# Optimization experiments

Measured on AMD Instinct MI355X. Metric: run time of the kernel, lower is better.

## Reference

```python
import jax, jax.numpy as jnp
import numpy as np

EPS = 1e-5  # torch BatchNorm1d default eps


def setup_inputs() -> dict:
    key = jax.random.key(0)
    ks = jax.random.split(key, 8)
    F, P = 32, 64            # frames, peds per frame
    B = F * P                # batch = 2048
    E, H, M, D = 64, 128, 512, 1024  # embed, h_dim, pool_mlp_dim, bottleneck
    starts = np.arange(F, dtype=np.int64) * P
    seq_start_end = jnp.asarray(np.stack([starts, starts + P], axis=1))
    inp = {
        "curr_h_states": jax.random.normal(ks[0], (1, B, H), dtype=jnp.float32),
        "curr_pos": jax.random.normal(ks[1], (B, 2), dtype=jnp.float32),
        "seq_start_end": seq_start_end,
        # embedding: Linear(2, E)
        "We": jax.random.normal(ks[2], (2, E), dtype=jnp.float32) * 0.5,
        "be": jnp.zeros((E,), dtype=jnp.float32),
        # mlp layer 1: Linear(E+H, M) + BN(M)
        "W1": jax.random.normal(ks[3], (E + H, M), dtype=jnp.float32) * 0.05,
        "b1": jnp.zeros((M,), dtype=jnp.float32),
        "g1": jnp.ones((M,), dtype=jnp.float32),
        "beta1": jnp.zeros((M,), dtype=jnp.float32),
        # mlp layer 2: Linear(M, D) + BN(D)
        "W2": jax.random.normal(ks[4], (M, D), dtype=jnp.float32) * 0.04,
        "b2": jnp.zeros((D,), dtype=jnp.float32),
        "g2": jnp.ones((D,), dtype=jnp.float32),
        "beta2": jnp.zeros((D,), dtype=jnp.float32),
        # BN running stats (eval mode)
        "rm1": jnp.zeros((M,), dtype=jnp.float32),
        "rv1": jnp.ones((M,), dtype=jnp.float32),
        "rm2": jnp.zeros((D,), dtype=jnp.float32),
        "rv2": jnp.ones((D,), dtype=jnp.float32),
    }
    return inp


def _bn(x, g, beta, rm, rv):
    return g * (x - rm) * jax.lax.rsqrt(rv + EPS) + beta


def reference(curr_h_states, curr_pos, seq_start_end, We, be, W1, b1, g1, beta1,
              W2, b2, g2, beta2, rm1, rv1, rm2, rv2):
    # Equal-size frames: vectorize the per-frame Python loop via a reshape.
    F = seq_start_end.shape[0]
    B = curr_h_states.shape[1]
    P = B // F
    h = curr_h_states[0].reshape(F, P, -1)      # (F, P, H)
    pos = curr_pos.reshape(F, P, 2)             # (F, P, 2)
    # rel_pos[f, i, j] = pos[f, j] - pos[f, i]  (repeat minus repeat_interleave)
    rel = pos[:, None, :, :] - pos[:, :, None, :]          # (F, P, P, 2)
    emb = rel @ We + be                                     # (F, P, P, E)
    h_rep = jnp.broadcast_to(h[:, None, :, :], (F, P, P, h.shape[-1]))
    x = jnp.concatenate([emb, h_rep], axis=-1)              # (F, P, P, E+H)
    x = jax.nn.relu(_bn(x @ W1 + b1, g1, beta1, rm1, rv1))  # (F, P, P, M)
    x = jax.nn.relu(_bn(x @ W2 + b2, g2, beta2, rm2, rv2))  # (F, P, P, D)
    pool_h = x.max(axis=2)                                  # max over j -> (F, P, D)
    return pool_h.reshape(B, -1)                            # (B, D)
```

## Files before the change

kernel.cpp:

```cpp
#include <hip/hip_runtime.h>
#include <hip/hip_bf16.h>
#include <stdint.h>

#define EPS_BN 1e-5f

constexpr int Fn = 32;
constexpr int Pn = 64;
constexpr int Bn = 2048;
constexpr int Hn = 128;
constexpr int En = 64;
constexpr int Mn = 512;
constexpr int Dn = 1024;

using bf16x8  = __attribute__((ext_vector_type(8))) short;
using f32x16  = __attribute__((ext_vector_type(16))) float;

static __device__ __forceinline__ float    bcf(uint32_t u) { return __builtin_bit_cast(float, u); }
static __device__ __forceinline__ uint32_t bcu(float f)    { return __builtin_bit_cast(uint32_t, f); }
static __device__ __forceinline__ unsigned short bfbits(float f) {
  return __builtin_bit_cast(unsigned short, __float2bfloat16(f));
}

static __device__ __forceinline__ void dma16(const uint4* g, uint4* l) {
  __builtin_amdgcn_global_load_lds(
      (const __attribute__((address_space(1))) unsigned int*)g,
      (__attribute__((address_space(3))) unsigned int*)l, 16, 0, 0);
}

static __device__ __forceinline__ bf16x8 mk_af(uint4 a, uint4 q) {
  uint4 x;
#pragma unroll
  for (int v = 0; v < 4; ++v) {
    uint32_t aw = ((const uint32_t*)&a)[v], qw = ((const uint32_t*)&q)[v];
    float lo = fmaxf(bcf(aw << 16) - bcf(qw << 16), 0.f);
    float hi = fmaxf(bcf(aw) - bcf(qw), 0.f);
    ((uint32_t*)&x)[v] = __builtin_amdgcn_perm(bcu(hi), bcu(lo), 0x07060302u);
  }
  return __builtin_bit_cast(bf16x8, x);
}

__global__ void prep_all(const float* __restrict__ hs, const float* __restrict__ pos,
                         const float* __restrict__ We, const float* __restrict__ be,
                         const float* __restrict__ W1, const float* __restrict__ b1,
                         const float* __restrict__ g1, const float* __restrict__ beta1,
                         const float* __restrict__ rm1, const float* __restrict__ rv1,
                         const float* __restrict__ W2, const float* __restrict__ b2,
                         const float* __restrict__ g2, const float* __restrict__ beta2,
                         const float* __restrict__ rm2, const float* __restrict__ rv2,
                         __hip_bfloat16* __restrict__ Agb, __hip_bfloat16* __restrict__ Qgb,
                         uint4* __restrict__ W2g, float* __restrict__ c2) {
  __shared__ float smem[64 * 65];
  int bid = blockIdx.x, t = threadIdx.x;
  if (bid < 512) {
    int rb = bid * 4, m = t;
    float* hsh = smem;
    float* psh = smem + 512;
    if (t < 4 * Hn) hsh[t] = hs[rb * Hn + t];
    if (t < 8) psh[t] = pos[rb * 2 + t];
    __syncthreads();
    float w0 = 0.f, w1 = 0.f, c = 0.f;
    for (int e = 0; e < En; ++e) {
      float w = W1[e * Mn + m];
      w0 += We[e] * w; w1 += We[En + e] * w; c += be[e] * w;
    }
    c += b1[m];
    float s  = g1[m] * rsqrtf(rv1[m] + EPS_BN);
    float tt = beta1[m] - rm1[m] * s;
    float acc[4];
#pragma unroll
    for (int ri = 0; ri < 4; ++ri) acc[ri] = c;
    for (int e = 0; e < Hn; ++e) {
      float w = W1[(En + e) * Mn + m];
#pragma unroll
      for (int ri = 0; ri < 4; ++ri) acc[ri] += hsh[ri * Hn + e] * w;
    }
#pragma unroll
    for (int ri = 0; ri < 4; ++ri) {
      float q = psh[ri * 2] * w0 + psh[ri * 2 + 1] * w1;
      Agb[(rb + ri) * Mn + m] = __float2bfloat16((acc[ri] + q) * s + tt);
      Qgb[(rb + ri) * Mn + m] = __float2bfloat16(q * s);
    }
  } else {
    int b2i = bid - 512;
    int d0 = (b2i & 15) * 64, k0 = (b2i >> 4) * 64;
    int col = t & 63, row8 = t >> 6;
#pragma unroll
    for (int rr = 0; rr < 8; ++rr) {
      int row = rr * 8 + row8;
      smem[row * 65 + col] = W2[(k0 + row) * Dn + d0 + col];
    }
    __syncthreads();
    int lane = t & 63, q8 = t >> 6;
    int sel_n = q8 & 1, sel_ks = q8 >> 1;
    int dl = sel_n * 32 + (lane & 31), d = d0 + dl;
    float sf = g2[d] * rsqrtf(rv2[d] + EPS_BN);
    int kb = sel_ks * 16 + (lane >> 5) * 8;
    uint32_t wd[4];
#pragma unroll
    for (int h = 0; h < 4; ++h) {
      uint32_t u0 = bfbits(smem[(kb + 2 * h) * 65 + dl] * sf);
      uint32_t u1 = bfbits(smem[(kb + 2 * h + 1) * 65 + dl] * sf);
      wd[h] = u0 | (u1 << 16);
    }
    int n32 = (d0 >> 5) + sel_n;
    int ks  = (k0 >> 4) + sel_ks;
    W2g[(n32 * 32 + ks) * 64 + lane] = (uint4){wd[0], wd[1], wd[2], wd[3]};
    if (k0 == 0 && t < 64) {
      int dd = d0 + t;
      float ss = g2[dd] * rsqrtf(rv2[dd] + EPS_BN);
      c2[dd] = b2[dd] * ss + beta2[dd] - rm2[dd] * ss;
    }
  }
}

__launch_bounds__(256, 2)
__global__ void gemm_pool(const __hip_bfloat16* __restrict__ Agb,
                          const __hip_bfloat16* __restrict__ Qgb,
                          const uint4* __restrict__ W2g,
                          const float* __restrict__ c2, float* __restrict__ out) {
  __shared__ uint4 Bs[4096];

  int ct = blockIdx.x;
  int rt = blockIdx.y;
  int f = rt >> 4, i0 = (rt & 15) * 4;

  int t = threadIdx.x, lane = t & 63, w = t >> 6;
  int i = i0 + w;
  int ko = lane >> 5;

  const uint4* aPj0 = (const uint4*)(Agb + (f * Pn + (lane & 31)) * Mn) + ko;
  const uint4* aPj1 = (const uint4*)(Agb + (f * Pn + 32 + (lane & 31)) * Mn) + ko;
  const uint4* qP   = (const uint4*)(Qgb + (f * Pn + i) * Mn) + ko;
  const uint4* W2base = W2g + (size_t)(4 * ct) * 32 * 64 + lane;

  f32x16 acc[2][4];
#pragma unroll
  for (int jf = 0; jf < 2; ++jf)
#pragma unroll
    for (int nf = 0; nf < 4; ++nf)
      acc[jf][nf] = (f32x16){0.f,0.f,0.f,0.f,0.f,0.f,0.f,0.f,0.f,0.f,0.f,0.f,0.f,0.f,0.f,0.f};

  uint4 rA00 = aPj0[0], rA01 = aPj1[0], rQ0 = qP[0];
  uint4 rA10 = aPj0[2], rA11 = aPj1[2], rQ1 = qP[2];

  for (int ph = 0; ph < 2; ++ph) {
    if (ph) __syncthreads();
#pragma unroll
    for (int s = 0; s < 16; ++s) {
      int slot = w * 16 + s;
      int ksl = slot >> 2, nf = slot & 3;
      dma16(W2base + (nf * 32 + ph * 16 + ksl) * 64, Bs + slot * 64);
    }
    __syncthreads();

    for (int kc8 = 0; kc8 < 8; ++kc8) {
      int kc = ph * 8 + kc8;
      int kn = (kc < 15) ? kc + 1 : 15;
      {
        bf16x8 af0 = mk_af(rA00, rQ0);
        bf16x8 af1 = mk_af(rA01, rQ0);
#pragma unroll
        for (int nf = 0; nf < 4; ++nf) {
          bf16x8 bg = *(const bf16x8*)(Bs + ((kc8 * 2 + 0) * 4 + nf) * 64 + lane);
          acc[0][nf] = __builtin_amdgcn_mfma_f32_32x32x16_bf16(af0, bg, acc[0][nf], 0, 0, 0);
          acc[1][nf] = __builtin_amdgcn_mfma_f32_32x32x16_bf16(af1, bg, acc[1][nf], 0, 0, 0);
        }
      }
      rA00 = aPj0[kn * 4]; rA01 = aPj1[kn * 4]; rQ0 = qP[kn * 4];
      {
        bf16x8 af0 = mk_af(rA10, rQ1);
        bf16x8 af1 = mk_af(rA11, rQ1);
#pragma unroll
        for (int nf = 0; nf < 4; ++nf) {
          bf16x8 bg = *(const bf16x8*)(Bs + ((kc8 * 2 + 1) * 4 + nf) * 64 + lane);
          acc[0][nf] = __builtin_amdgcn_mfma_f32_32x32x16_bf16(af0, bg, acc[0][nf], 0, 0, 0);
          acc[1][nf] = __builtin_amdgcn_mfma_f32_32x32x16_bf16(af1, bg, acc[1][nf], 0, 0, 0);
        }
      }
      rA10 = aPj0[kn * 4 + 2]; rA11 = aPj1[kn * 4 + 2]; rQ1 = qP[kn * 4 + 2];
    }
  }

#pragma unroll
  for (int nf = 0; nf < 4; ++nf) {
    float mx = 0.f;
#pragma unroll
    for (int jf = 0; jf < 2; ++jf)
#pragma unroll
      for (int rg = 0; rg < 16; ++rg)
        mx = fmaxf(mx, acc[jf][nf][rg]);
    mx = fmaxf(mx, __shfl_xor(mx, 32));
    if (lane < 32) {
      int d = ct * 128 + nf * 32 + (lane & 31);
      out[(f * Pn + i) * Dn + d] = fmaxf(mx + c2[d], 0.f);
    }
  }
}

extern "C" void kernel_launch(void* const* d_in, const int* in_sizes, int n_in,
                              void* d_out, int out_size, void* d_ws, size_t ws_size,
                              hipStream_t stream) {
  const float* hs    = (const float*)d_in[0];
  const float* pos   = (const float*)d_in[1];
  const float* We    = (const float*)d_in[3];
  const float* be    = (const float*)d_in[4];
  const float* W1    = (const float*)d_in[5];
  const float* b1    = (const float*)d_in[6];
  const float* g1    = (const float*)d_in[7];
  const float* beta1 = (const float*)d_in[8];
  const float* W2    = (const float*)d_in[9];
  const float* b2    = (const float*)d_in[10];
  const float* g2    = (const float*)d_in[11];
  const float* beta2 = (const float*)d_in[12];
  const float* rm1   = (const float*)d_in[13];
  const float* rv1   = (const float*)d_in[14];
  const float* rm2   = (const float*)d_in[15];
  const float* rv2   = (const float*)d_in[16];

  char* ws = (char*)d_ws;
  float* c2 = (float*)(ws + 0);
  __hip_bfloat16* Agb = (__hip_bfloat16*)(ws + 4096);
  __hip_bfloat16* Qgb = (__hip_bfloat16*)(ws + 4096 + 2097152);
  uint4* W2g = (uint4*)(ws + 4096 + 2 * 2097152);
  float* out = (float*)d_out;

  prep_all<<<640, 512, 0, stream>>>(hs, pos, We, be, W1, b1, g1, beta1, rm1, rv1,
                                    W2, b2, g2, beta2, rm2, rv2, Agb, Qgb, W2g, c2);
  gemm_pool<<<dim3(Dn / 128, (Fn * Pn * Pn) / 256), 256, 0, stream>>>(Agb, Qgb, W2g, c2, out);
}
```

Measured before the change: 264.6 us.

## Stage shared A rows in LDS and split W2 loads into four phases

After: 250.5 us. 5.3% less time.

```diff
diff --git a/kernel.cpp b/kernel.cpp
--- a/kernel.cpp
+++ b/kernel.cpp
@@ -21,7 +21,7 @@
   return __builtin_bit_cast(unsigned short, __float2bfloat16(f));
 }
 
-static __device__ __forceinline__ void dma16(const uint4* g, uint4* l) {
+static __device__ __forceinline__ void dma16(const uint4* g, const uint4* l) {
   __builtin_amdgcn_global_load_lds(
       (const __attribute__((address_space(1))) unsigned int*)g,
       (__attribute__((address_space(3))) unsigned int*)l, 16, 0, 0);
@@ -118,7 +118,7 @@
                           const __hip_bfloat16* __restrict__ Qgb,
                           const uint4* __restrict__ W2g,
                           const float* __restrict__ c2, float* __restrict__ out) {
-  __shared__ uint4 Bs[4096];
+  __shared__ uint4 SH[4096];
 
   int ct = blockIdx.x;
   int rt = blockIdx.y;
@@ -126,12 +126,25 @@
 
   int t = threadIdx.x, lane = t & 63, w = t >> 6;
   int i = i0 + w;
-  int ko = lane >> 5;
-
-  const uint4* aPj0 = (const uint4*)(Agb + (f * Pn + (lane & 31)) * Mn) + ko;
-  const uint4* aPj1 = (const uint4*)(Agb + (f * Pn + 32 + (lane & 31)) * Mn) + ko;
-  const uint4* qP   = (const uint4*)(Qgb + (f * Pn + i) * Mn) + ko;
-  const uint4* W2base = W2g + (size_t)(4 * ct) * 32 * 64 + lane;
+
+  const uint4* Au4 = (const uint4*)(Agb + (size_t)f * Pn * Mn);
+  const uint4* aGL = Au4 + (size_t)(lane & 31) * 64 + (lane >> 5);
+  const uint4* bGL = W2g + (size_t)(4 * ct) * 32 * 64 + lane;
+  const uint4* qP = (const uint4*)(Qgb + (size_t)(f * Pn + i) * Mn) + (lane >> 5);
+
+#pragma unroll
+  for (int s = 0; s < 8; ++s) {
+    int sa = w * 8 + s;
+    int kcA = sa >> 2, kst = (sa >> 1) & 1, jf = sa & 1;
+    dma16(aGL + (size_t)jf * 32 * 64 + kcA * 4 + kst * 2, SH + sa * 64);
+  }
+#pragma unroll
+  for (int s = 0; s < 8; ++s) {
+    int sb = w * 8 + s;
+    int kq = sb >> 2, nf = sb & 3;
+    dma16(bGL + (nf * 32 + kq) * 64, SH + 2048 + sb * 64);
+  }
+  uint4 qc0 = qP[0], qc1 = qP[2];
 
   f32x16 acc[2][4];
 #pragma unroll
@@ -140,44 +153,50 @@
     for (int nf = 0; nf < 4; ++nf)
       acc[jf][nf] = (f32x16){0.f,0.f,0.f,0.f,0.f,0.f,0.f,0.f,0.f,0.f,0.f,0.f,0.f,0.f,0.f,0.f};
 
-  uint4 rA00 = aPj0[0], rA01 = aPj1[0], rQ0 = qP[0];
-  uint4 rA10 = aPj0[2], rA11 = aPj1[2], rQ1 = qP[2];
-
-  for (int ph = 0; ph < 2; ++ph) {
-    if (ph) __syncthreads();
-#pragma unroll
-    for (int s = 0; s < 16; ++s) {
-      int slot = w * 16 + s;
-      int ksl = slot >> 2, nf = slot & 3;
-      dma16(W2base + (nf * 32 + ph * 16 + ksl) * 64, Bs + slot * 64);
-    }
-    __syncthreads();
-
-    for (int kc8 = 0; kc8 < 8; ++kc8) {
-      int kc = ph * 8 + kc8;
+  __syncthreads();
+
+#pragma unroll
+  for (int sp = 0; sp < 4; ++sp) {
+    if (sp) {
+      __syncthreads();
+      if (sp == 2) {
+#pragma unroll
+        for (int s = 0; s < 8; ++s) {
+          int sa = w * 8 + s;
+          int kcA = sa >> 2, kst = (sa >> 1) & 1, jf = sa & 1;
+          dma16(aGL + (size_t)jf * 32 * 64 + (kcA + 8) * 4 + kst * 2, SH + sa * 64);
+        }
+      }
+#pragma unroll
+      for (int s = 0; s < 8; ++s) {
+        int sb = w * 8 + s;
+        int kq = sb >> 2, nf = sb & 3;
+        dma16(bGL + (nf * 32 + sp * 8 + kq) * 64, SH + 2048 + sb * 64);
+      }
+      __syncthreads();
+    }
+#pragma unroll
+    for (int kcl = 0; kcl < 4; ++kcl) {
+      int kc = sp * 4 + kcl;
       int kn = (kc < 15) ? kc + 1 : 15;
-      {
-        bf16x8 af0 = mk_af(rA00, rQ0);
-        bf16x8 af1 = mk_af(rA01, rQ0);
+      uint4 qn0 = qP[kn * 4], qn1 = qP[kn * 4 + 2];
+#pragma unroll
+      for (int kst = 0; kst < 2; ++kst) {
+        int aBase = (((kc & 7) * 2 + kst) * 2) * 64 + lane;
+        uint4 a0 = SH[aBase];
+        uint4 a1 = SH[aBase + 64];
+        int bBase = 2048 + ((kcl * 2 + kst) * 4) * 64 + lane;
+        uint4 q = kst ? qc1 : qc0;
+        bf16x8 af0 = mk_af(a0, q);
+        bf16x8 af1 = mk_af(a1, q);
 #pragma unroll
         for (int nf = 0; nf < 4; ++nf) {
-          bf16x8 bg = *(const bf16x8*)(Bs + ((kc8 * 2 + 0) * 4 + nf) * 64 + lane);
+          bf16x8 bg = *(const bf16x8*)(SH + bBase + nf * 64);
           acc[0][nf] = __builtin_amdgcn_mfma_f32_32x32x16_bf16(af0, bg, acc[0][nf], 0, 0, 0);
           acc[1][nf] = __builtin_amdgcn_mfma_f32_32x32x16_bf16(af1, bg, acc[1][nf], 0, 0, 0);
         }
       }
-      rA00 = aPj0[kn * 4]; rA01 = aPj1[kn * 4]; rQ0 = qP[kn * 4];
-      {
-        bf16x8 af0 = mk_af(rA10, rQ1);
-        bf16x8 af1 = mk_af(rA11, rQ1);
-#pragma unroll
-        for (int nf = 0; nf < 4; ++nf) {
-          bf16x8 bg = *(const bf16x8*)(Bs + ((kc8 * 2 + 1) * 4 + nf) * 64 + lane);
-          acc[0][nf] = __builtin_amdgcn_mfma_f32_32x32x16_bf16(af0, bg, acc[0][nf], 0, 0, 0);
-          acc[1][nf] = __builtin_amdgcn_mfma_f32_32x32x16_bf16(af1, bg, acc[1][nf], 0, 0, 0);
-        }
-      }
-      rA10 = aPj0[kn * 4 + 2]; rA11 = aPj1[kn * 4 + 2]; rQ1 = qP[kn * 4 + 2];
+      qc0 = qn0; qc1 = qn1;
     }
   }
 
```
